# Kernel optimization log

Measured on AMD Instinct MI355X. Metric: run time of the kernel, lower is better.

Reference implementation:

```python
import jax, jax.numpy as jnp
import numpy as np

N = 100000        # nodes
E = 1600000       # edges (avg degree 16)
IN = 128          # in_channels
HID = 256         # hidden_channels
OUT = 2           # out_channels
G = 512           # num graphs in batch


def setup_inputs() -> dict:
    key = jax.random.key(0)
    ks = jax.random.split(key, 10)
    x = jax.random.normal(ks[0], (N, IN), dtype=jnp.float32)
    edge_index = jax.random.randint(ks[1], (2, E), 0, N, dtype=jnp.int64)
    # sorted graph assignment, every graph non-empty (PyG-style batching)
    batch = (jnp.arange(N, dtype=jnp.int64) * G) // N
    s = 1.0 / np.sqrt(IN)
    sh = 1.0 / np.sqrt(2 * HID)
    sh1 = 1.0 / np.sqrt(HID)
    W_l = jax.random.uniform(ks[2], (HID, IN), jnp.float32, -s, s)   # SAGE lin_l (neighbors)
    b_l = jax.random.uniform(ks[3], (HID,), jnp.float32, -s, s)
    W_r = jax.random.uniform(ks[4], (HID, IN), jnp.float32, -s, s)   # SAGE lin_r (root), no bias
    W0 = jax.random.uniform(ks[5], (HID, IN), jnp.float32, -s, s)    # lin0
    b0 = jax.random.uniform(ks[5], (HID,), jnp.float32, -s, s)
    W1 = jax.random.uniform(ks[6], (HID, 2 * HID), jnp.float32, -sh, sh)  # lin1
    b1 = jax.random.uniform(ks[7], (HID,), jnp.float32, -sh, sh)
    W2 = jax.random.uniform(ks[8], (OUT, HID), jnp.float32, -sh1, sh1)    # lin2
    b2 = jax.random.uniform(ks[9], (OUT,), jnp.float32, -sh1, sh1)
    return {"x": x, "edge_index": edge_index, "batch": batch,
            "W_l": W_l, "b_l": b_l, "W_r": W_r,
            "W0": W0, "b0": b0, "W1": W1, "b1": b1, "W2": W2, "b2": b2}


def reference(x, edge_index, batch, W_l, b_l, W_r, W0, b0, W1, b1, W2, b2):
    src, dst = edge_index[0], edge_index[1]
    # SAGEConv: mean-aggregate neighbor features (gather -> scatter-add -> normalize)
    msg_sum = jax.ops.segment_sum(x[src], dst, num_segments=N)          # [N, IN]
    deg = jax.ops.segment_sum(jnp.ones((E,), x.dtype), dst, num_segments=N)
    aggr = msg_sum / jnp.maximum(deg, 1.0)[:, None]
    h = jax.nn.relu(aggr @ W_l.T + b_l + x @ W_r.T)                     # [N, HID]
    # global max pool per graph
    hp = jax.ops.segment_max(h, batch, num_segments=G)                  # [G, HID]
    # root node = first node of each graph (batch is sorted)
    root = jnp.searchsorted(batch, jnp.arange(G, dtype=batch.dtype))    # [G]
    news = jax.nn.relu(x[root] @ W0.T + b0)                             # [G, HID]
    h = jax.nn.relu(jnp.concatenate([news, hp], axis=-1) @ W1.T + b1)   # [G, HID]
    h = h @ W2.T + b2                                                   # [G, OUT]
    return jax.nn.log_softmax(h, axis=-1)
```

## Files before the change

kernel.cpp:

```cpp
#include <hip/hip_runtime.h>
#include <hip/hip_bf16.h>
#include <math.h>
#include <stdint.h>

#define IN_C 128
#define HID  256
#define OUT_C 2

#define BSHIFT 8
#define BNODES 256
#define EPB 8192
#define HISTB 784
#define PADB 768

typedef __attribute__((ext_vector_type(8))) short short8;
typedef __attribute__((ext_vector_type(4))) float f32x4;
typedef __attribute__((ext_vector_type(2))) float f32x2;

#if defined(__has_builtin)
#if __has_builtin(__builtin_amdgcn_cvt_pk_f32_fp8) && __has_builtin(__builtin_amdgcn_cvt_pk_fp8_f32)
#define HAVE_FP8_CVT 1
#endif
#if __has_builtin(__builtin_amdgcn_global_load_lds)
#define HAVE_GLL 1
#endif
#endif

__device__ __forceinline__ ushort f2bf(float f) {
  uint32_t u = __float_as_uint(f);
  uint32_t r = u + 0x7FFF + ((u >> 16) & 1);
  return (ushort)(r >> 16);
}
__device__ __forceinline__ float bf2f(ushort b) {
  return __uint_as_float(((uint32_t)b) << 16);
}

#ifndef HAVE_FP8_CVT
__device__ __forceinline__ uint32_t f2fp8_1(float f) {
  uint32_t u = __float_as_uint(f);
  uint32_t s = (u >> 24) & 0x80;
  float a = fabsf(f);
  if (a >= 448.f) return s | 0x7E;
  if (a < 0.015625f) {
    uint32_t m = (uint32_t)(a * 512.f + 0.5f);
    return s | m;
  }
  uint32_t r = u & 0x7fffffff;
  r += 0x7FFFF + ((r >> 20) & 1);
  uint32_t e = (r >> 23) - 127;
  if ((int)e > 8) return s | 0x7E;
  return s | ((e + 7) << 3) | ((r >> 20) & 7);
}
__device__ __forceinline__ float fp8_2f(uint32_t b) {
  uint32_t s = (b & 0x80) << 24;
  uint32_t e = (b >> 3) & 0xF, m = b & 7;
  if (e == 0) { float f = (float)m * 0.001953125f; return s ? -f : f; }
  return __uint_as_float(s | ((e + 120) << 23) | (m << 20));
}
#endif

__device__ __forceinline__ void acc8f8v(f32x2* s, uint2 v) {
#ifdef HAVE_FP8_CVT
  s[0] += __builtin_amdgcn_cvt_pk_f32_fp8(v.x, false);
  s[1] += __builtin_amdgcn_cvt_pk_f32_fp8(v.x, true);
  s[2] += __builtin_amdgcn_cvt_pk_f32_fp8(v.y, false);
  s[3] += __builtin_amdgcn_cvt_pk_f32_fp8(v.y, true);
#else
  s[0].x += fp8_2f(v.x & 0xff);         s[0].y += fp8_2f((v.x >> 8) & 0xff);
  s[1].x += fp8_2f((v.x >> 16) & 0xff); s[1].y += fp8_2f(v.x >> 24);
  s[2].x += fp8_2f(v.y & 0xff);         s[2].y += fp8_2f((v.y >> 8) & 0xff);
  s[3].x += fp8_2f((v.y >> 16) & 0xff); s[3].y += fp8_2f(v.y >> 24);
#endif
}


__global__ void k_prep(const float* __restrict__ x, ushort* __restrict__ xb,
                       uint32_t* __restrict__ xf8, int n4,
                       const float* __restrict__ Wl, const float* __restrict__ Wr,
                       ushort* __restrict__ Wcat,
                       const float* __restrict__ W0, ushort* __restrict__ W0b,
                       const float* __restrict__ W1, ushort* __restrict__ W1b,
                       const int* __restrict__ batch, int* __restrict__ root, int n,
                       const int* __restrict__ dst, int E, int* __restrict__ bcount,
                       float* __restrict__ hp, int hp4) {
  __shared__ int h[512];
  int t = threadIdx.x;
  int i = blockIdx.x * 256 + t;
  if (i < n4) {
    float4 v = ((const float4*)x)[i];
    ushort4 o = {f2bf(v.x), f2bf(v.y), f2bf(v.z), f2bf(v.w)};
    ((ushort4*)xb)[i] = o;
#ifdef HAVE_FP8_CVT
    int p = __builtin_amdgcn_cvt_pk_fp8_f32(v.x, v.y, 0, false);
    p = __builtin_amdgcn_cvt_pk_fp8_f32(v.z, v.w, p, true);
    xf8[i] = (uint32_t)p;
#else
    xf8[i] = f2fp8_1(v.x) | (f2fp8_1(v.y) << 8) | (f2fp8_1(v.z) << 16) |
             (f2fp8_1(v.w) << 24);
#endif
  }
  if (i < 32) xf8[(size_t)n * 32 + i] = 0;
  if (i < HID * (2 * IN_C) / 4) {
    int c = i >> 6, c4 = (i & 63) * 4;
    float4 v = (c4 < IN_C) ? *(const float4*)(Wl + (size_t)c * IN_C + c4)
                           : *(const float4*)(Wr + (size_t)c * IN_C + (c4 - IN_C));
    ushort4 o = {f2bf(v.x), f2bf(v.y), f2bf(v.z), f2bf(v.w)};
    *(ushort4*)(Wcat + (size_t)c * (2 * IN_C) + c4) = o;
  }
  if (i < HID * IN_C / 4) {
    float4 v = ((const float4*)W0)[i];
    ushort4 o = {f2bf(v.x), f2bf(v.y), f2bf(v.z), f2bf(v.w)};
    ((ushort4*)W0b)[i] = o;
  }
  if (i < HID * 2 * HID / 4) {
    float4 v = ((const float4*)W1)[i];
    ushort4 o = {f2bf(v.x), f2bf(v.y), f2bf(v.z), f2bf(v.w)};
    ((ushort4*)W1b)[i] = o;
  }
  if (i < hp4) ((float4*)hp)[i] = make_float4(0.f, 0.f, 0.f, 0.f);
  if (i < n) {
    int g = batch[i];
    if (i == 0 || batch[i - 1] != g) root[g] = i;
  }
  if (blockIdx.x < HISTB) {
    h[t] = 0; h[t + 256] = 0;
    __syncthreads();
    for (int e = blockIdx.x * 256 + t; e < E; e += HISTB * 256)
      atomicAdd(&h[dst[e] >> BSHIFT], 1);
    __syncthreads();
    if (h[t]) atomicAdd(&bcount[t], h[t]);
    if (h[t + 256]) atomicAdd(&bcount[t + 256], h[t + 256]);
  }
}


__global__ __launch_bounds__(256) void k_scatter(
    const int* __restrict__ src, const int* __restrict__ dst,
    const int* __restrict__ bcount, int* __restrict__ cursor0,
    uint32_t* __restrict__ rec, int E) {
  __shared__ int sBB[512];
  __shared__ int stmp[256];
  __shared__ int h[512];
  __shared__ int hb[512];
  __shared__ int lcur[512];
  int t = threadIdx.x;
  int c0 = bcount[2 * t], c1 = bcount[2 * t + 1];
  stmp[t] = c0 + c1;
  h[2 * t] = 0; h[2 * t + 1] = 0;
  lcur[2 * t] = 0; lcur[2 * t + 1] = 0;
  __syncthreads();
  for (int off = 1; off < 256; off <<= 1) {
    int v = (t >= off) ? stmp[t - off] : 0;
    __syncthreads();
    stmp[t] += v;
    __syncthreads();
  }
  int ex = stmp[t] - (c0 + c1);
  sBB[2 * t] = ex;
  sBB[2 * t + 1] = ex + c0;
  __syncthreads();

  int e0 = blockIdx.x * EPB;
  int e1 = e0 + EPB < E ? e0 + EPB : E;
  for (int e = e0 + t; e < e1; e += 256)
    atomicAdd(&h[dst[e] >> BSHIFT], 1);
  __syncthreads();
  for (int j = t; j < 512; j += 256)
    if (h[j]) hb[j] = sBB[j] + atomicAdd(&cursor0[j], h[j]);
  __syncthreads();
  for (int e = e0 + t; e < e1; e += 256) {
    int d = dst[e];
    int b = d >> BSHIFT;
    int r = atomicAdd(&lcur[b], 1);
    rec[hb[b] + r] = ((uint32_t)src[e] << BSHIFT) | ((uint32_t)d & (BNODES - 1));
  }
}


__global__ __launch_bounds__(256) void k_csr(
    const uint32_t* __restrict__ rec, const int* __restrict__ bcount,
    int* __restrict__ row_start, int* __restrict__ deg,
    int* __restrict__ csr, int n, int zrow) {
  __shared__ int stmp[256];
  __shared__ int lexcl[256];
  __shared__ int ldeg[256];
  __shared__ int lcur[256];
  int t = threadIdx.x, b = blockIdx.x;
  int i2 = 2 * t;
  int v = ((i2 < b) ? bcount[i2] : 0) + ((i2 + 1 < b) ? bcount[i2 + 1] : 0);
  stmp[t] = v;
  ldeg[t] = 0;
  __syncthreads();
  for (int off = 128; off > 0; off >>= 1) {
    if (t < off) stmp[t] += stmp[t + off];
    __syncthreads();
  }
  int ebase = stmp[0];
  int ecnt = bcount[b];
  int padbase = ((ebase + 3) & ~3) + PADB * b;
  int node0 = b << BSHIFT;
  __syncthreads();

  for (int i = t; i < ecnt; i += 256)
    atomicAdd(&ldeg[rec[ebase + i] & (BNODES - 1)], 1);
  __syncthreads();
  int d = ldeg[t];
  int P = (d + 3) & ~3;
  stmp[t] = P;
  __syncthreads();
  for (int off = 1; off < 256; off <<= 1) {
    int vv = (t >= off) ? stmp[t - off] : 0;
    __syncthreads();
    stmp[t] += vv;
    __syncthreads();
  }
  int excl = stmp[t] - P;
  lexcl[t] = excl;
  int rs = padbase + excl;
  int node = node0 + t;
  if (node < n) { row_start[node] = rs; deg[node] = d; }
  lcur[t] = 0;
  __syncthreads();
  for (int i = t; i < ecnt; i += 256) {
    uint32_t r = rec[ebase + i];
    int li = r & (BNODES - 1);
    int k = atomicAdd(&lcur[li], 1);
    csr[padbase + lexcl[li] + k] = (int)(r >> BSHIFT);
  }
  for (int k = d; k < P; ++k) csr[rs + k] = zrow;
}


__global__ void k_aggr(const uint32_t* __restrict__ xf8, const int* __restrict__ csr,
                       const int* __restrict__ row_start, const int* __restrict__ deg,
                       ushort* __restrict__ aggr, int n) {
  int wid = threadIdx.x >> 6;
  int lane = threadIdx.x & 63;
  int q = lane >> 4, li = lane & 15;
  int node = blockIdx.x * 16 + wid * 4 + q;
  bool alive = node < n;
  int base = alive ? row_start[node] : 0;
  int d = alive ? deg[node] : 0;
  int P = (d + 3) & ~3;
  const uint2* xp = (const uint2*)xf8 + li;
  f32x2 s[4] = {};
  for (int i = 0; i < P; i += 4) {
    int4 ns = *(const int4*)(csr + base + i);
    uint2 a = xp[(size_t)ns.x * 16];
    uint2 b = xp[(size_t)ns.y * 16];
    uint2 c = xp[(size_t)ns.z * 16];
    uint2 e = xp[(size_t)ns.w * 16];
    acc8f8v(s, a); acc8f8v(s, b); acc8f8v(s, c); acc8f8v(s, e);
  }
  if (alive) {
    float inv = 1.0f / (float)(d > 1 ? d : 1);
    uint4 o;
    o.x = (uint32_t)f2bf(s[0].x * inv) | ((uint32_t)f2bf(s[0].y * inv) << 16);
    o.y = (uint32_t)f2bf(s[1].x * inv) | ((uint32_t)f2bf(s[1].y * inv) << 16);
    o.z = (uint32_t)f2bf(s[2].x * inv) | ((uint32_t)f2bf(s[2].y * inv) << 16);
    o.w = (uint32_t)f2bf(s[3].x * inv) | ((uint32_t)f2bf(s[3].y * inv) << 16);
    ((uint4*)(aggr + (size_t)node * IN_C))[li] = o;
  }
}


#ifdef HAVE_GLL
__device__ __forceinline__ void load16_lds(const ushort* g, ushort* l) {
  __builtin_amdgcn_global_load_lds(
      (const __attribute__((address_space(1))) uint32_t*)g,
      (__attribute__((address_space(3))) uint32_t*)l, 16, 0, 0);
}
#endif

__global__ __launch_bounds__(256) void k_gemm_pool(
    const ushort* __restrict__ aggrb, const ushort* __restrict__ xb,
    const ushort* __restrict__ Wcat, const float* __restrict__ bl,
    const int* __restrict__ batch, float* __restrict__ hp, int n) {
  __shared__ ushort sA[64 * 256];
  __shared__ float sbl[256];
  __shared__ int sBatch[64];

  int t = threadIdx.x;
  int n0 = blockIdx.x * 64;
  sbl[t] = bl[t];
  if (t < 64) sBatch[t] = (n0 + t < n) ? batch[n0 + t] : -1;

  int lane = t & 63, w = t >> 6;
  int q = lane >> 4, m = lane & 15;

#pragma unroll
  for (int j = 0; j < 8; ++j) {
    int s = (j * 4 + w) * 64 + lane;
    int r = s >> 5, p = s & 31;
    int c = p ^ (r & 15);
    int gn = n0 + r; gn = gn < n ? gn : n - 1;
    const ushort* g = (c < 16) ? aggrb + (size_t)gn * IN_C + c * 8
                               : xb + (size_t)gn * IN_C + (c - 16) * 8;
#ifdef HAVE_GLL
    load16_lds(g, &sA[(size_t)s * 8]);
#else
    *(uint4*)&sA[(size_t)s * 8] = *(const uint4*)g;
#endif
  }

  short8 bf_n[4];
#pragma unroll
  for (int ct = 0; ct < 4; ++ct)
    bf_n[ct] = *(const short8*)(Wcat + (size_t)(w * 64 + ct * 16 + m) * (2 * IN_C) + q * 8);

  __syncthreads();

  f32x4 acc[4][4] = {};
#pragma unroll
  for (int kc = 0; kc < 8; ++kc) {
    short8 bf[4];
#pragma unroll
    for (int ct = 0; ct < 4; ++ct) bf[ct] = bf_n[ct];
    if (kc < 7) {
#pragma unroll
      for (int ct = 0; ct < 4; ++ct)
        bf_n[ct] = *(const short8*)(Wcat + (size_t)(w * 64 + ct * 16 + m) * (2 * IN_C) +
                                    (kc + 1) * 32 + q * 8);
    }
    short8 af[4];
#pragma unroll
    for (int rt = 0; rt < 4; ++rt) {
      int r = rt * 16 + m;
      int p = (kc * 4 + q) ^ m;
      af[rt] = *(const short8*)&sA[r * 256 + p * 8];
    }
#pragma unroll
    for (int rt = 0; rt < 4; ++rt)
#pragma unroll
      for (int ct = 0; ct < 4; ++ct)
        acc[rt][ct] = __builtin_amdgcn_mfma_f32_16x16x32_bf16(af[rt], bf[ct], acc[rt][ct], 0, 0, 0);
  }

  int last = n - 1 - n0; last = last < 63 ? last : 63;
  int gA = sBatch[0];
  int gB = sBatch[last];
#pragma unroll
  for (int ct = 0; ct < 4; ++ct) {
    int col = w * 64 + ct * 16 + m;
    float bias = sbl[col];
    float mA = 0.f, mB = 0.f;
#pragma unroll
    for (int rt = 0; rt < 4; ++rt) {
#pragma unroll
      for (int i = 0; i < 4; ++i) {
        int lr = rt * 16 + q * 4 + i;
        if (n0 + lr < n) {
          float v = fmaxf(acc[rt][ct][i] + bias, 0.f);
          if (sBatch[lr] == gA) mA = fmaxf(mA, v);
          else mB = fmaxf(mB, v);
        }
      }
    }
    mA = fmaxf(mA, __shfl_xor(mA, 16)); mA = fmaxf(mA, __shfl_xor(mA, 32));
    mB = fmaxf(mB, __shfl_xor(mB, 16)); mB = fmaxf(mB, __shfl_xor(mB, 32));
    if (q == 0) {
      atomicMax((int*)&hp[(size_t)gA * HID + col], __float_as_int(mA));
      if (gB != gA) atomicMax((int*)&hp[(size_t)gB * HID + col], __float_as_int(mB));
    }
  }
}


__global__ __launch_bounds__(256) void k_tail(
    const ushort* __restrict__ xb, const float* __restrict__ hp,
    const int* __restrict__ root,
    const ushort* __restrict__ W0b, const float* __restrict__ b0,
    const ushort* __restrict__ W1b, const float* __restrict__ b1,
    const float* __restrict__ W2, const float* __restrict__ b2,
    float* __restrict__ out, int G) {
  __shared__ ushort sCat[32][264];
  __shared__ int sRoot[32];
  __shared__ float pp[256][2];

  int t = threadIdx.x;
  int g0 = blockIdx.x * 32;
  if (t < 32) sRoot[t] = (g0 + t < G) ? root[g0 + t] : 0;
  __syncthreads();

  int lane = t & 63, w = t >> 6;
  int q = lane >> 4, m = lane & 15;

  const ushort* xrow[2];
#pragma unroll
  for (int rt = 0; rt < 2; ++rt)
    xrow[rt] = xb + (size_t)sRoot[rt * 16 + m] * IN_C;

  {
    f32x4 acc[2][4] = {};
#pragma unroll
    for (int kc = 0; kc < 4; ++kc) {
      short8 af[2], bf[4];
#pragma unroll
      for (int rt = 0; rt < 2; ++rt)
        af[rt] = *(const short8*)(xrow[rt] + kc * 32 + q * 8);
#pragma unroll
      for (int ct = 0; ct < 4; ++ct) {
        int col = w * 64 + ct * 16 + m;
        bf[ct] = *(const short8*)(W0b + (size_t)col * IN_C + kc * 32 + q * 8);
      }
#pragma unroll
      for (int rt = 0; rt < 2; ++rt)
#pragma unroll
        for (int ct = 0; ct < 4; ++ct)
          acc[rt][ct] = __builtin_amdgcn_mfma_f32_16x16x32_bf16(af[rt], bf[ct], acc[rt][ct], 0, 0, 0);
    }
#pragma unroll
    for (int ct = 0; ct < 4; ++ct) {
      int col = w * 64 + ct * 16 + m;
      float bias = b0[col];
#pragma unroll
      for (int rt = 0; rt < 2; ++rt)
#pragma unroll
        for (int i = 0; i < 4; ++i) {
          int row = rt * 16 + q * 4 + i;
          sCat[row][col] = f2bf(fmaxf(acc[rt][ct][i] + bias, 0.f));
        }
    }
  }
  __syncthreads();

  f32x4 acc2[2][4] = {};
  short8 bfn[4];
#pragma unroll
  for (int ct = 0; ct < 4; ++ct)
    bfn[ct] = *(const short8*)(W1b + (size_t)(w * 64 + ct * 16 + m) * (2 * HID) + q * 8);
#pragma unroll
  for (int kc = 0; kc < 8; ++kc) {
    short8 af[2], bf[4];
#pragma unroll
    for (int ct = 0; ct < 4; ++ct) bf[ct] = bfn[ct];
    if (kc < 7) {
#pragma unroll
      for (int ct = 0; ct < 4; ++ct)
        bfn[ct] = *(const short8*)(W1b + (size_t)(w * 64 + ct * 16 + m) * (2 * HID) +
                                   (kc + 1) * 32 + q * 8);
    }
#pragma unroll
    for (int rt = 0; rt < 2; ++rt)
      af[rt] = *(const short8*)&sCat[rt * 16 + m][kc * 32 + q * 8];
#pragma unroll
    for (int rt = 0; rt < 2; ++rt)
#pragma unroll
      for (int ct = 0; ct < 4; ++ct)
        acc2[rt][ct] = __builtin_amdgcn_mfma_f32_16x16x32_bf16(af[rt], bf[ct], acc2[rt][ct], 0, 0, 0);
  }
  __syncthreads();
#pragma unroll
  for (int it = 0; it < 8; ++it) {
    int idx = it * 256 + t;
    int r = idx >> 6, c4 = (idx & 63) * 4;
    if (g0 + r < G) {
      float4 v = *(const float4*)(hp + (size_t)(g0 + r) * HID + c4);
      ushort4 o = {f2bf(v.x), f2bf(v.y), f2bf(v.z), f2bf(v.w)};
      *(ushort4*)&sCat[r][c4] = o;
    }
  }
  __syncthreads();
#pragma unroll
  for (int ct = 0; ct < 4; ++ct)
    bfn[ct] = *(const short8*)(W1b + (size_t)(w * 64 + ct * 16 + m) * (2 * HID) + 8 * 32 + q * 8);
#pragma unroll
  for (int kc = 8; kc < 16; ++kc) {
    short8 af[2], bf[4];
#pragma unroll
    for (int ct = 0; ct < 4; ++ct) bf[ct] = bfn[ct];
    if (kc < 15) {
#pragma unroll
      for (int ct = 0; ct < 4; ++ct)
        bfn[ct] = *(const short8*)(W1b + (size_t)(w * 64 + ct * 16 + m) * (2 * HID) +
                                   (kc + 1) * 32 + q * 8);
    }
#pragma unroll
    for (int rt = 0; rt < 2; ++rt)
      af[rt] = *(const short8*)&sCat[rt * 16 + m][(kc - 8) * 32 + q * 8];
#pragma unroll
    for (int rt = 0; rt < 2; ++rt)
#pragma unroll
      for (int ct = 0; ct < 4; ++ct)
        acc2[rt][ct] = __builtin_amdgcn_mfma_f32_16x16x32_bf16(af[rt], bf[ct], acc2[rt][ct], 0, 0, 0);
  }
  __syncthreads();
#pragma unroll
  for (int ct = 0; ct < 4; ++ct) {
    int col = w * 64 + ct * 16 + m;
    float bias = b1[col];
#pragma unroll
    for (int rt = 0; rt < 2; ++rt)
#pragma unroll
      for (int i = 0; i < 4; ++i) {
        int row = rt * 16 + q * 4 + i;
        sCat[row][col] = f2bf(fmaxf(acc2[rt][ct][i] + bias, 0.f));
      }
  }
  __syncthreads();

  {
    int row = t >> 3, qq = t & 7;
    float p0 = 0.f, p1 = 0.f;
    for (int c = qq * 32; c < qq * 32 + 32; ++c) {
      float hv = bf2f(sCat[row][c]);
      p0 += hv * W2[c];
      p1 += hv * W2[HID + c];
    }
    pp[t][0] = p0; pp[t][1] = p1;
  }
  __syncthreads();
  if (t < 32 && g0 + t < G) {
    float l0 = b2[0], l1 = b2[1];
#pragma unroll
    for (int k = 0; k < 8; ++k) { l0 += pp[t * 8 + k][0]; l1 += pp[t * 8 + k][1]; }
    float mx = fmaxf(l0, l1);
    float ls = logf(expf(l0 - mx) + expf(l1 - mx));
    out[(size_t)(g0 + t) * 2 + 0] = l0 - mx - ls;
    out[(size_t)(g0 + t) * 2 + 1] = l1 - mx - ls;
  }
}


extern "C" void kernel_launch(void* const* d_in, const int* in_sizes, int n_in,
                              void* d_out, int out_size, void* d_ws, size_t ws_size,
                              hipStream_t stream) {
  const float* x  = (const float*)d_in[0];
  const int* ei   = (const int*)d_in[1];
  const int* batch= (const int*)d_in[2];
  const float* Wl = (const float*)d_in[3];
  const float* bl = (const float*)d_in[4];
  const float* Wr = (const float*)d_in[5];
  const float* W0 = (const float*)d_in[6];
  const float* b0 = (const float*)d_in[7];
  const float* W1 = (const float*)d_in[8];
  const float* b1 = (const float*)d_in[9];
  const float* W2 = (const float*)d_in[10];
  const float* b2 = (const float*)d_in[11];
  float* out = (float*)d_out;

  const int N = in_sizes[0] / IN_C;
  const int E = in_sizes[1] / 2;
  const int G = out_size / OUT_C;
  const int* src = ei;
  const int* dst = ei + E;
  const int NB = (N + BNODES - 1) >> BSHIFT;

  char* w = (char*)d_ws;
  int* deg       = (int*)w; w += (size_t)N * 4;
  int* row_start = (int*)w; w += (size_t)N * 4;
  int* bcount    = (int*)w; w += 2048;
  int* cursor0   = (int*)w; w += 2048;
  int* root      = (int*)w; w += (size_t)G * 4;
  w = (char*)(((uintptr_t)w + 255) & ~(uintptr_t)255);
  int* csr       = (int*)w; w += (size_t)(E + PADB * NB + 8192) * 4;
  w = (char*)(((uintptr_t)w + 255) & ~(uintptr_t)255);
  ushort* xb     = (ushort*)w; w += (size_t)N * IN_C * 2;
  uint32_t* xf8  = (uint32_t*)w; w += (size_t)(N + 1) * IN_C;
  ushort* aggrb  = (ushort*)w; w += (size_t)N * IN_C * 2;
  ushort* Wcat   = (ushort*)w; w += (size_t)HID * (2 * IN_C) * 2;
  ushort* W0b    = (ushort*)w; w += (size_t)HID * IN_C * 2;
  ushort* W1b    = (ushort*)w; w += (size_t)HID * 2 * HID * 2;
  float* hp      = (float*)w; w += (size_t)G * HID * 4;
  uint32_t* rec  = (uint32_t*)aggrb;

  hipMemsetAsync(bcount, 0, 4096, stream);

  int n4 = N * IN_C / 4;
  k_prep<<<(n4 + 255) / 256, 256, 0, stream>>>(
      x, xb, xf8, n4, Wl, Wr, Wcat, W0, W0b, W1, W1b, batch, root, N,
      dst, E, bcount, hp, G * HID / 4);
  k_scatter<<<(E + EPB - 1) / EPB, 256, 0, stream>>>(src, dst, bcount, cursor0, rec, E);
  k_csr<<<NB, 256, 0, stream>>>(rec, bcount, row_start, deg, csr, N, N);
  k_aggr<<<(N + 15) / 16, 256, 0, stream>>>(xf8, csr, row_start, deg, aggrb, N);
  k_gemm_pool<<<(N + 63) / 64, 256, 0, stream>>>(aggrb, xb, Wcat, bl, batch, hp, N);
  k_tail<<<(G + 31) / 32, 256, 0, stream>>>(xb, hp, root, W0b, b0, W1b, b1, W2, b2, out, G);
}
```

Baseline: 278.7 us.

## Vectorize edge loads in CSR build and load GEMM A-tiles directly from global

Halves the edges handled per scatter block, and switches the histogram, scatter and CSR passes to read dst/src/rec four at a time with int4/uint4 loads, adding scalar tail loops. The pooled GEMM no longer stages the activation tile in LDS via global_load_lds. Each wave now loads its A fragments straight from global memory with register prefetch, so every wave re-reads the same A rows. This trades LDS footprint and a barrier for redundant global or L2 traffic. The vector loads assume 16-byte aligned arrays and per-block offsets.

```diff
diff --git a/kernel.cpp b/kernel.cpp
--- a/kernel.cpp
+++ b/kernel.cpp
@@ -9,7 +9,7 @@
 
 #define BSHIFT 8
 #define BNODES 256
-#define EPB 8192
+#define EPB 4096
 #define HISTB 784
 #define PADB 768
 
@@ -20,9 +20,6 @@
 #if defined(__has_builtin)
 #if __has_builtin(__builtin_amdgcn_cvt_pk_f32_fp8) && __has_builtin(__builtin_amdgcn_cvt_pk_fp8_f32)
 #define HAVE_FP8_CVT 1
-#endif
-#if __has_builtin(__builtin_amdgcn_global_load_lds)
-#define HAVE_GLL 1
 #endif
 #endif
 
@@ -125,8 +122,18 @@
   if (blockIdx.x < HISTB) {
     h[t] = 0; h[t + 256] = 0;
     __syncthreads();
-    for (int e = blockIdx.x * 256 + t; e < E; e += HISTB * 256)
-      atomicAdd(&h[dst[e] >> BSHIFT], 1);
+    int E4 = E >> 2;
+    const int4* d4 = (const int4*)dst;
+    for (int e = blockIdx.x * 256 + t; e < E4; e += HISTB * 256) {
+      int4 d = d4[e];
+      atomicAdd(&h[d.x >> BSHIFT], 1);
+      atomicAdd(&h[d.y >> BSHIFT], 1);
+      atomicAdd(&h[d.z >> BSHIFT], 1);
+      atomicAdd(&h[d.w >> BSHIFT], 1);
+    }
+    if (blockIdx.x == 0)
+      for (int e = (E4 << 2) + t; e < E; e += 256)
+        atomicAdd(&h[dst[e] >> BSHIFT], 1);
     __syncthreads();
     if (h[t]) atomicAdd(&bcount[t], h[t]);
     if (h[t + 256]) atomicAdd(&bcount[t + 256], h[t + 256]);
@@ -162,17 +169,49 @@
 
   int e0 = blockIdx.x * EPB;
   int e1 = e0 + EPB < E ? e0 + EPB : E;
-  for (int e = e0 + t; e < e1; e += 256)
-    atomicAdd(&h[dst[e] >> BSHIFT], 1);
+  int cnt = e1 - e0;
+  int cnt4 = cnt >> 2;
+  const int4* d4 = (const int4*)(dst + e0);
+  const int4* s4 = (const int4*)(src + e0);
+
+  for (int i = t; i < cnt4; i += 256) {
+    int4 d = d4[i];
+    atomicAdd(&h[d.x >> BSHIFT], 1);
+    atomicAdd(&h[d.y >> BSHIFT], 1);
+    atomicAdd(&h[d.z >> BSHIFT], 1);
+    atomicAdd(&h[d.w >> BSHIFT], 1);
+  }
+  for (int i = (cnt4 << 2) + t; i < cnt; i += 256)
+    atomicAdd(&h[dst[e0 + i] >> BSHIFT], 1);
   __syncthreads();
   for (int j = t; j < 512; j += 256)
     if (h[j]) hb[j] = sBB[j] + atomicAdd(&cursor0[j], h[j]);
   __syncthreads();
-  for (int e = e0 + t; e < e1; e += 256) {
-    int d = dst[e];
+  for (int i = t; i < cnt4; i += 256) {
+    int4 d = d4[i];
+    int4 s = s4[i];
+    {
+      int b = d.x >> BSHIFT; int r = atomicAdd(&lcur[b], 1);
+      rec[hb[b] + r] = ((uint32_t)s.x << BSHIFT) | ((uint32_t)d.x & (BNODES - 1));
+    }
+    {
+      int b = d.y >> BSHIFT; int r = atomicAdd(&lcur[b], 1);
+      rec[hb[b] + r] = ((uint32_t)s.y << BSHIFT) | ((uint32_t)d.y & (BNODES - 1));
+    }
+    {
+      int b = d.z >> BSHIFT; int r = atomicAdd(&lcur[b], 1);
+      rec[hb[b] + r] = ((uint32_t)s.z << BSHIFT) | ((uint32_t)d.z & (BNODES - 1));
+    }
+    {
+      int b = d.w >> BSHIFT; int r = atomicAdd(&lcur[b], 1);
+      rec[hb[b] + r] = ((uint32_t)s.w << BSHIFT) | ((uint32_t)d.w & (BNODES - 1));
+    }
+  }
+  for (int i = (cnt4 << 2) + t; i < cnt; i += 256) {
+    int d = dst[e0 + i];
     int b = d >> BSHIFT;
     int r = atomicAdd(&lcur[b], 1);
-    rec[hb[b] + r] = ((uint32_t)src[e] << BSHIFT) | ((uint32_t)d & (BNODES - 1));
+    rec[hb[b] + r] = ((uint32_t)src[e0 + i] << BSHIFT) | ((uint32_t)d & (BNODES - 1));
   }
 }
 
@@ -201,8 +240,17 @@
   int node0 = b << BSHIFT;
   __syncthreads();
 
-  for (int i = t; i < ecnt; i += 256)
-    atomicAdd(&ldeg[rec[ebase + i] & (BNODES - 1)], 1);
+  const uint32_t* rb = rec + ebase;
+  int ec4 = ecnt >> 2;
+  for (int i = t; i < ec4; i += 256) {
+    uint4 r = *(const uint4*)(rb + i * 4);
+    atomicAdd(&ldeg[r.x & (BNODES - 1)], 1);
+    atomicAdd(&ldeg[r.y & (BNODES - 1)], 1);
+    atomicAdd(&ldeg[r.z & (BNODES - 1)], 1);
+    atomicAdd(&ldeg[r.w & (BNODES - 1)], 1);
+  }
+  for (int i = (ec4 << 2) + t; i < ecnt; i += 256)
+    atomicAdd(&ldeg[rb[i] & (BNODES - 1)], 1);
   __syncthreads();
   int d = ldeg[t];
   int P = (d + 3) & ~3;
@@ -221,8 +269,27 @@
   if (node < n) { row_start[node] = rs; deg[node] = d; }
   lcur[t] = 0;
   __syncthreads();
-  for (int i = t; i < ecnt; i += 256) {
-    uint32_t r = rec[ebase + i];
+  for (int i = t; i < ec4; i += 256) {
+    uint4 r = *(const uint4*)(rb + i * 4);
+    {
+      int li = r.x & (BNODES - 1); int k = atomicAdd(&lcur[li], 1);
+      csr[padbase + lexcl[li] + k] = (int)(r.x >> BSHIFT);
+    }
+    {
+      int li = r.y & (BNODES - 1); int k = atomicAdd(&lcur[li], 1);
+      csr[padbase + lexcl[li] + k] = (int)(r.y >> BSHIFT);
+    }
+    {
+      int li = r.z & (BNODES - 1); int k = atomicAdd(&lcur[li], 1);
+      csr[padbase + lexcl[li] + k] = (int)(r.z >> BSHIFT);
+    }
+    {
+      int li = r.w & (BNODES - 1); int k = atomicAdd(&lcur[li], 1);
+      csr[padbase + lexcl[li] + k] = (int)(r.w >> BSHIFT);
+    }
+  }
+  for (int i = (ec4 << 2) + t; i < ecnt; i += 256) {
+    uint32_t r = rb[i];
     int li = r & (BNODES - 1);
     int k = atomicAdd(&lcur[li], 1);
     csr[padbase + lexcl[li] + k] = (int)(r >> BSHIFT);
@@ -264,19 +331,10 @@
 }
 
 
-#ifdef HAVE_GLL
-__device__ __forceinline__ void load16_lds(const ushort* g, ushort* l) {
-  __builtin_amdgcn_global_load_lds(
-      (const __attribute__((address_space(1))) uint32_t*)g,
-      (__attribute__((address_space(3))) uint32_t*)l, 16, 0, 0);
-}
-#endif
-
 __global__ __launch_bounds__(256) void k_gemm_pool(
     const ushort* __restrict__ aggrb, const ushort* __restrict__ xb,
     const ushort* __restrict__ Wcat, const float* __restrict__ bl,
     const int* __restrict__ batch, float* __restrict__ hp, int n) {
-  __shared__ ushort sA[64 * 256];
   __shared__ float sbl[256];
   __shared__ int sBatch[64];
 
@@ -284,50 +342,47 @@
   int n0 = blockIdx.x * 64;
   sbl[t] = bl[t];
   if (t < 64) sBatch[t] = (n0 + t < n) ? batch[n0 + t] : -1;
+  __syncthreads();
 
   int lane = t & 63, w = t >> 6;
   int q = lane >> 4, m = lane & 15;
 
-#pragma unroll
-  for (int j = 0; j < 8; ++j) {
-    int s = (j * 4 + w) * 64 + lane;
-    int r = s >> 5, p = s & 31;
-    int c = p ^ (r & 15);
-    int gn = n0 + r; gn = gn < n ? gn : n - 1;
-    const ushort* g = (c < 16) ? aggrb + (size_t)gn * IN_C + c * 8
-                               : xb + (size_t)gn * IN_C + (c - 16) * 8;
-#ifdef HAVE_GLL
-    load16_lds(g, &sA[(size_t)s * 8]);
-#else
-    *(uint4*)&sA[(size_t)s * 8] = *(const uint4*)g;
-#endif
-  }
-
-  short8 bf_n[4];
+  const ushort* arow[4];
+  const ushort* xrow[4];
+  const ushort* wrow[4];
+#pragma unroll
+  for (int rt = 0; rt < 4; ++rt) {
+    int gn = n0 + rt * 16 + m; gn = gn < n ? gn : n - 1;
+    arow[rt] = aggrb + (size_t)gn * IN_C + q * 8;
+    xrow[rt] = xb + (size_t)gn * IN_C + q * 8;
+  }
 #pragma unroll
   for (int ct = 0; ct < 4; ++ct)
-    bf_n[ct] = *(const short8*)(Wcat + (size_t)(w * 64 + ct * 16 + m) * (2 * IN_C) + q * 8);
-
-  __syncthreads();
+    wrow[ct] = Wcat + (size_t)(w * 64 + ct * 16 + m) * (2 * IN_C) + q * 8;
+
+  short8 afn[4], bfn[4];
+#pragma unroll
+  for (int rt = 0; rt < 4; ++rt) afn[rt] = *(const short8*)arow[rt];
+#pragma unroll
+  for (int ct = 0; ct < 4; ++ct) bfn[ct] = *(const short8*)wrow[ct];
 
   f32x4 acc[4][4] = {};
 #pragma unroll
   for (int kc = 0; kc < 8; ++kc) {
-    short8 bf[4];
-#pragma unroll
-    for (int ct = 0; ct < 4; ++ct) bf[ct] = bf_n[ct];
+    short8 af[4], bf[4];
+#pragma unroll
+    for (int rt = 0; rt < 4; ++rt) af[rt] = afn[rt];
+#pragma unroll
+    for (int ct = 0; ct < 4; ++ct) bf[ct] = bfn[ct];
     if (kc < 7) {
+      int kn = kc + 1;
+#pragma unroll
+      for (int rt = 0; rt < 4; ++rt)
+        afn[rt] = (kn < 4) ? *(const short8*)(arow[rt] + kn * 32)
+                           : *(const short8*)(xrow[rt] + (kn - 4) * 32);
 #pragma unroll
       for (int ct = 0; ct < 4; ++ct)
-        bf_n[ct] = *(const short8*)(Wcat + (size_t)(w * 64 + ct * 16 + m) * (2 * IN_C) +
-                                    (kc + 1) * 32 + q * 8);
-    }
-    short8 af[4];
-#pragma unroll
-    for (int rt = 0; rt < 4; ++rt) {
-      int r = rt * 16 + m;
-      int p = (kc * 4 + q) ^ m;
-      af[rt] = *(const short8*)&sA[r * 256 + p * 8];
+        bfn[ct] = *(const short8*)(wrow[ct] + kn * 32);
     }
 #pragma unroll
     for (int rt = 0; rt < 4; ++rt)
```

New measurement: 283.7 us. Within noise of the previous version (+1.8%).
